# Kernel tuning notes

Hardware: AMD Instinct MI355X
Metric: run time of the kernel (lower is better)

The kernel has to match this reference:

```python
import jax, jax.numpy as jnp
import numpy as np

EPS = 1e-5
N_HEADS = 4

def _ln(x, s, b):
    m = x.mean(-1, keepdims=True)
    v = ((x - m) ** 2).mean(-1, keepdims=True)
    return (x - m) / jnp.sqrt(v + EPS) * s + b

def _gelu(x):
    return jax.nn.gelu(x, approximate=False)  # torch nn.GELU default (erf)


def setup_inputs() -> dict:
    key = jax.random.key(0)
    ks = jax.random.split(key, 20)
    H, AF, BF, DEPTH = 256, 153, 14, 4
    n_mols, apm = 1024, 48
    n_atoms = n_mols * apm          # 49152
    max_nb = 6
    n_bonds = 3 * n_atoms           # 147456 directed bonds
    def nrm(k, shape, scale=0.02):
        return jax.random.normal(k, shape, jnp.float32) * scale
    return dict(
        f_atoms=jax.random.normal(ks[0], (n_atoms, AF), jnp.float32),
        f_bonds=jax.random.normal(ks[1], (n_bonds, BF), jnp.float32),
        a2b=jax.random.randint(ks[2], (n_atoms, max_nb), 0, n_bonds),
        b2a=jax.random.randint(ks[3], (n_bonds,), 0, n_atoms),
        b2revb=jax.random.randint(ks[4], (n_bonds,), 0, n_bonds),
        W_i=nrm(ks[5], (AF + BF, H)), b_i=jnp.zeros((H,), jnp.float32),
        W_h=nrm(ks[6], (DEPTH - 1, H, H)), b_h=jnp.zeros((DEPTH - 1, H), jnp.float32),
        ln_msg_s=jnp.ones((DEPTH - 1, H), jnp.float32), ln_msg_b=jnp.zeros((DEPTH - 1, H), jnp.float32),
        W_o=nrm(ks[7], (AF + H, H)), b_o=jnp.zeros((H,), jnp.float32),
        ln_atom_s=jnp.ones((H,), jnp.float32), ln_atom_b=jnp.zeros((H,), jnp.float32),
        q_w=nrm(ks[8], (H, H)), q_b=jnp.zeros((H,), jnp.float32),
        k_w=nrm(ks[9], (H, H)), k_b=jnp.zeros((H,), jnp.float32),
        v_w=nrm(ks[10], (H, H)), v_b=jnp.zeros((H,), jnp.float32),
        o_w=nrm(ks[11], (H, H)), o_b=jnp.zeros((H,), jnp.float32),
        ln1_s=jnp.ones((H,), jnp.float32), ln1_b=jnp.zeros((H,), jnp.float32),
        ln2_s=jnp.ones((H,), jnp.float32), ln2_b=jnp.zeros((H,), jnp.float32),
        ff1_w=nrm(ks[12], (H, 2 * H)), ff1_b=jnp.zeros((2 * H,), jnp.float32),
        ff2_w=nrm(ks[13], (2 * H, H)), ff2_b=jnp.zeros((H,), jnp.float32),
        readout_query=nrm(ks[14], (1, 1, H)),
        rk_w=nrm(ks[15], (H, H)), rk_b=jnp.zeros((H,), jnp.float32),
        n_mols=n_mols, atoms_per_mol=apm,
    )


def reference(f_atoms, f_bonds, a2b, b2a, b2revb,
              W_i, b_i, W_h, b_h, ln_msg_s, ln_msg_b, W_o, b_o,
              ln_atom_s, ln_atom_b, q_w, q_b, k_w, k_b, v_w, v_b, o_w, o_b,
              ln1_s, ln1_b, ln2_s, ln2_b, ff1_w, ff1_b, ff2_w, ff2_b,
              readout_query, rk_w, rk_b, n_mols, atoms_per_mol):
    H = W_i.shape[1]
    HD = H // N_HEADS
    depth = W_h.shape[0] + 1

    # ---- D-MPNN message passing over directed bonds ----
    message = _gelu(jnp.concatenate([f_atoms[b2a], f_bonds], axis=1) @ W_i + b_i)  # [n_bonds,H]
    for t in range(depth - 1):  # fixed small depth loop
        nei = message[a2b].sum(axis=1)                 # [n_atoms,H] gather-sum over incoming bonds
        nei_m = nei[b2a] - message[b2revb]             # [n_bonds,H] subtract reverse bond
        message = message + _gelu(_ln(nei_m, ln_msg_s[t], ln_msg_b[t]) @ W_h[t] + b_h[t])

    a_message = message[a2b].sum(axis=1)               # [n_atoms,H]
    atom_h = _gelu(jnp.concatenate([f_atoms, a_message], axis=1) @ W_o + b_o)
    atom_h = _ln(atom_h, ln_atom_s, ln_atom_b)

    # uniform scopes: padding loop becomes a reshape, mask is all-valid
    x = atom_h.reshape(n_mols, atoms_per_mol, H)

    # ---- pre-norm TransformerEncoderLayer ----
    h = _ln(x, ln1_s, ln1_b)
    def heads(t):
        return t.reshape(n_mols, atoms_per_mol, N_HEADS, HD).transpose(0, 2, 1, 3)
    q = heads(h @ q_w + q_b)
    k = heads(h @ k_w + k_b)
    v = heads(h @ v_w + v_b)
    attn = jax.nn.softmax(jnp.einsum('bhqd,bhkd->bhqk', q, k) / float(np.sqrt(HD)), axis=-1)
    ctx = jnp.einsum('bhqk,bhkd->bhqd', attn, v).transpose(0, 2, 1, 3).reshape(n_mols, atoms_per_mol, H)
    x = x + (ctx @ o_w + o_b)
    h2 = _ln(x, ln2_s, ln2_b)
    x = x + (_gelu(h2 @ ff1_w + ff1_b) @ ff2_w + ff2_b)

    # ---- attention-weighted readout ----
    keys = x @ rk_w + rk_b                             # [B,S,H]
    scores = jnp.einsum('bsh,h->bs', keys, readout_query[0, 0])
    w = jax.nn.softmax(scores, axis=-1)[..., None]
    return (x * w).sum(axis=1)                         # [B,H]
```

## Files before the change

kernel.cpp:

```cpp
#include <hip/hip_runtime.h>
#include <hip/hip_bf16.h>
#include <math.h>

#define H 256
#define AFEAT 153
#define BFEAT 14
#define KINIT 167
#define NA 49152
#define NB 147456
#define NMOL 1024
#define APM 48
#define MAXNB 6
#define NHEAD 4
#define HDIM 64
#define EPSLN 1e-5f
#define KI_PAD 192
#define KO_PAD 448

typedef unsigned short u16;
typedef __attribute__((ext_vector_type(8))) short bf16x8;
typedef __attribute__((ext_vector_type(4))) short bf16x4;
typedef __attribute__((ext_vector_type(4))) float f32x4;

__device__ __forceinline__ float gelu_f(float x) {
    return 0.5f * x * (1.0f + erff(x * 0.70710678118654752f));
}
__device__ __forceinline__ float wave_sum(float v) {
    #pragma unroll
    for (int m = 1; m < 64; m <<= 1) v += __shfl_xor(v, m);
    return v;
}
__device__ __forceinline__ float b2f(u16 u) {
    union { unsigned u32; float f; } c; c.u32 = ((unsigned)u) << 16; return c.f;
}
__device__ __forceinline__ u16 f2b(float f) {
    __hip_bfloat16 h = __float2bfloat16(f);
    u16 u; __builtin_memcpy(&u, &h, 2); return u;
}
__device__ __forceinline__ ushort4 f2b4(float a, float b, float c, float d) {
    ushort4 o; o.x = f2b(a); o.y = f2b(b); o.z = f2b(c); o.w = f2b(d); return o;
}
__device__ __forceinline__ unsigned addbf2(unsigned a, unsigned b) {
    float lo = b2f((u16)(a & 0xffff)) + b2f((u16)(b & 0xffff));
    float hi = b2f((u16)(a >> 16)) + b2f((u16)(b >> 16));
    return ((unsigned)f2b(hi) << 16) | (unsigned)f2b(lo);
}
__device__ __forceinline__ uint4 addbf8(uint4 a, uint4 b) {
    uint4 r;
    r.x = addbf2(a.x, b.x); r.y = addbf2(a.y, b.y);
    r.z = addbf2(a.z, b.z); r.w = addbf2(a.w, b.w);
    return r;
}

__device__ __forceinline__ f32x4 mfma16(bf16x4 a, bf16x4 b, f32x4 c) {
#if __has_builtin(__builtin_amdgcn_mfma_f32_16x16x16bf16_1k)
    return __builtin_amdgcn_mfma_f32_16x16x16bf16_1k(a, b, c, 0, 0, 0);
#elif __has_builtin(__builtin_amdgcn_mfma_f32_16x16x16_bf16_1k)
    return __builtin_amdgcn_mfma_f32_16x16x16_bf16_1k(a, b, c, 0, 0, 0);
#elif __has_builtin(__builtin_amdgcn_mfma_f32_16x16x16_bf16)
    return __builtin_amdgcn_mfma_f32_16x16x16_bf16(a, b, c, 0, 0, 0);
#else
    f32x4 d;
    asm("v_mfma_f32_16x16x16_bf16 %0, %1, %2, %3"
        : "=&v"(d) : "v"(a), "v"(b), "v"(c));
    return d;
#endif
}

typedef const __attribute__((address_space(1))) void* gas_ptr;
typedef __attribute__((address_space(3))) void* las_ptr;
__device__ __forceinline__ void gload_lds16(const u16* g, u16* l) {
    __builtin_amdgcn_global_load_lds((gas_ptr)g, (las_ptr)l, 16, 0, 0);
}

template<bool GELU, bool ACCUM>
__global__ __launch_bounds__(256) void gemm_mfma_k(
    const u16* __restrict__ A, int Ka,
    const u16* __restrict__ Wt,
    const float* __restrict__ bias,
    u16* __restrict__ C, int Nc, int K)
{
    __shared__ __align__(16) u16 S[128 * 128];
    u16* As = S;
    u16* Bs = S + 8192;
    const int tid = threadIdx.x;
    const int w = tid >> 6, l = tid & 63;
    const int r0 = blockIdx.x * 128;
    const int cb0 = blockIdx.y * 128;
    const int wr = (w >> 1) * 64;
    const int wc = (w & 1) * 64;

    f32x4 acc[4][4];
    #pragma unroll
    for (int m = 0; m < 4; ++m)
        #pragma unroll
        for (int n = 0; n < 4; ++n) acc[m][n] = (f32x4){0.f, 0.f, 0.f, 0.f};

    const int srow = l >> 3;
    const int ssrc = ((l & 7) * 16) ^ (srow << 4);
    const int fr = l & 15;
    const int fh = l >> 4;
    const int swz = (fr & 7) << 4;

    for (int k0 = 0; k0 < K; k0 += 64) {
        #pragma unroll
        for (int i = 0; i < 4; ++i) {
            const int seg = w * 4 + i;
            gload_lds16(A + (size_t)(r0 + seg * 8 + srow) * Ka + k0 + (ssrc >> 1),
                        &As[seg * 512]);
            gload_lds16(Wt + (size_t)(cb0 + seg * 8 + srow) * Ka + k0 + (ssrc >> 1),
                        &Bs[seg * 512]);
        }
        __syncthreads();
        #pragma unroll
        for (int s = 0; s < 2; ++s) {
            const int cbyte = ((s * 64 + fh * 16) ^ swz) >> 1;
            bf16x8 af[4], bv[4];
            #pragma unroll
            for (int m = 0; m < 4; ++m)
                af[m] = *(const bf16x8*)&As[(wr + m * 16 + fr) * 64 + cbyte];
            #pragma unroll
            for (int n = 0; n < 4; ++n)
                bv[n] = *(const bf16x8*)&Bs[(wc + n * 16 + fr) * 64 + cbyte];
            #pragma unroll
            for (int m = 0; m < 4; ++m)
                #pragma unroll
                for (int n = 0; n < 4; ++n)
                    acc[m][n] = __builtin_amdgcn_mfma_f32_16x16x32_bf16(
                        af[m], bv[n], acc[m][n], 0, 0, 0);
        }
        __syncthreads();
    }

    float bvv[4];
    #pragma unroll
    for (int n = 0; n < 4; ++n) bvv[n] = bias[cb0 + wc + n * 16 + fr];
    #pragma unroll
    for (int m = 0; m < 4; ++m)
        #pragma unroll
        for (int n = 0; n < 4; ++n) {
            const int col = wc + n * 16 + fr;
            #pragma unroll
            for (int j = 0; j < 4; ++j) {
                const int row = wr + m * 16 + fh * 4 + j;
                float v = acc[m][n][j] + bvv[n];
                if (GELU) v = gelu_f(v);
                *(u16*)((char*)S + row * 256 + ((col * 2) ^ ((row & 7) << 4))) = f2b(v);
            }
        }
    __syncthreads();
    {
        const int rrow = tid >> 1;
        const int rch = (tid & 1) * 128;
        const int rswz = (rrow & 7) << 4;
        u16* gp = C + (size_t)(r0 + rrow) * Nc + cb0 + (tid & 1) * 64;
        #pragma unroll
        for (int q = 0; q < 8; ++q) {
            uint4 dv = *(const uint4*)((const char*)S + rrow * 256 + ((rch + q * 16) ^ rswz));
            if (ACCUM) {
                uint4 ov = *(const uint4*)(gp + q * 8);
                dv = addbf8(dv, ov);
            }
            *(uint4*)(gp + q * 8) = dv;
        }
    }
}

struct LGather {
    const u16* nei; const u16* msg; const int* b2a; const int* b2revb;
    __device__ __forceinline__ float4 load4(int row, int lane) const {
        const int a = b2a[row], rv = b2revb[row];
        ushort4 un = *(const ushort4*)(nei + (size_t)a * H + lane * 4);
        ushort4 um = *(const ushort4*)(msg + (size_t)rv * H + lane * 4);
        return make_float4(b2f(un.x) - b2f(um.x), b2f(un.y) - b2f(um.y),
                           b2f(un.z) - b2f(um.z), b2f(un.w) - b2f(um.w));
    }
};
struct LPlain {
    const u16* X;
    __device__ __forceinline__ float4 load4(int row, int lane) const {
        ushort4 u = *(const ushort4*)(X + (size_t)row * H + lane * 4);
        return make_float4(b2f(u.x), b2f(u.y), b2f(u.z), b2f(u.w));
    }
};

template<class L, bool GELU, bool ACCUM>
__global__ __launch_bounds__(512, 4) void fln_gemm_k(
    L ld, const u16* __restrict__ Wt,
    const float* __restrict__ lns, const float* __restrict__ lnb,
    const float* __restrict__ bias,
    const u16* __restrict__ Cold,
    u16* __restrict__ C, int Nc)
{
    __shared__ __align__(16) u16 SH[64 * 256 + 256 * 64];
    u16* Alds = SH;
    u16* Blds = SH + 64 * 256;
    const int tid = threadIdx.x;
    const int w = tid >> 6, l = tid & 63;
    const int r0 = blockIdx.x * 64;
    const int cb0 = blockIdx.y * 256;
    const int fr = l & 15, fh = l >> 4;
    const int swzf = (fr & 7) << 4;

    {
        float4 sv = *(const float4*)(lns + l * 4);
        float4 bv = *(const float4*)(lnb + l * 4);
        #pragma unroll
        for (int i = 0; i < 8; ++i) {
            const int r = w * 8 + i;
            float4 v = ld.load4(r0 + r, l);
            float mean = wave_sum(v.x + v.y + v.z + v.w) * (1.0f / H);
            float dx = v.x - mean, dy = v.y - mean, dz = v.z - mean, dw = v.w - mean;
            float var = wave_sum(dx * dx + dy * dy + dz * dz + dw * dw) * (1.0f / H);
            float inv = rsqrtf(var + EPSLN);
            ushort4 o = f2b4(dx * inv * sv.x + bv.x, dy * inv * sv.y + bv.y,
                             dz * inv * sv.z + bv.z, dw * inv * sv.w + bv.w);
            *(ushort4*)((char*)&Alds[(size_t)r * 256] + ((l * 8) ^ ((r & 7) << 4))) = o;
        }
    }

    f32x4 acc[2][4];
    #pragma unroll
    for (int m = 0; m < 2; ++m)
        #pragma unroll
        for (int n = 0; n < 4; ++n) acc[m][n] = (f32x4){0.f, 0.f, 0.f, 0.f};

    const int wr = (w >> 2) * 32;
    const int wc = (w & 3) * 64;

    for (int kk = 0; kk < 4; ++kk) {
        #pragma unroll
        for (int i = 0; i < 4; ++i) {
            const int seg = w * 4 + i;
            const int n = seg * 8 + (l >> 3);
            const int sb = ((l & 7) * 16) ^ ((n & 7) << 4);
            gload_lds16(Wt + (size_t)(cb0 + n) * H + kk * 64 + (sb >> 1),
                        &Blds[seg * 512]);
        }
        __syncthreads();
        #pragma unroll
        for (int s = 0; s < 2; ++s) {
            bf16x8 af[2], bv[4];
            #pragma unroll
            for (int m = 0; m < 2; ++m)
                af[m] = *(const bf16x8*)((const char*)&Alds[(size_t)(wr + m * 16 + fr) * 256]
                        + ((kk * 128 + s * 64 + fh * 16) ^ swzf));
            #pragma unroll
            for (int n = 0; n < 4; ++n)
                bv[n] = *(const bf16x8*)((const char*)&Blds[(size_t)(wc + n * 16 + fr) * 64]
                        + ((s * 64 + fh * 16) ^ swzf));
            #pragma unroll
            for (int m = 0; m < 2; ++m)
                #pragma unroll
                for (int n = 0; n < 4; ++n)
                    acc[m][n] = __builtin_amdgcn_mfma_f32_16x16x32_bf16(
                        af[m], bv[n], acc[m][n], 0, 0, 0);
        }
        __syncthreads();
    }

    float bvv[4];
    #pragma unroll
    for (int n = 0; n < 4; ++n) bvv[n] = bias[cb0 + wc + n * 16 + fr];
    #pragma unroll
    for (int m = 0; m < 2; ++m)
        #pragma unroll
        for (int n = 0; n < 4; ++n) {
            const int col = wc + n * 16 + fr;
            #pragma unroll
            for (int j = 0; j < 4; ++j) {
                const int row = wr + m * 16 + fh * 4 + j;
                float v = acc[m][n][j] + bvv[n];
                if (GELU) v = gelu_f(v);
                *(u16*)((char*)&Alds[(size_t)row * 256] + ((col * 2) ^ ((row & 7) << 4))) = f2b(v);
            }
        }
    __syncthreads();
    {
        const int rrow = tid >> 3;
        const int rch = (tid & 7) * 64;
        const int rswz = (rrow & 7) << 4;
        u16* gp = C + (size_t)(r0 + rrow) * Nc + cb0 + (tid & 7) * 32;
        const u16* op = Cold + (size_t)(r0 + rrow) * Nc + cb0 + (tid & 7) * 32;
        #pragma unroll
        for (int q = 0; q < 4; ++q) {
            uint4 dv = *(const uint4*)((const char*)&Alds[(size_t)rrow * 256]
                        + ((rch + q * 16) ^ rswz));
            if (ACCUM) {
                uint4 ov = *(const uint4*)(op + q * 8);
                dv = addbf8(dv, ov);
            }
            *(uint4*)(gp + q * 8) = dv;
        }
    }
}

__global__ __launch_bounds__(256) void wcvt_k(const float* __restrict__ W,
    u16* __restrict__ Wt, int K, int N, int Kpad)
{
    int idx = blockIdx.x * 256 + threadIdx.x;
    if (idx >= N * Kpad) return;
    int n = idx / Kpad, kp = idx - n * Kpad;
    Wt[idx] = (kp < K) ? f2b(W[(size_t)kp * N + n]) : (u16)0;
}

__global__ void biaspack_k(const float* q, const float* k, const float* v, float* dst) {
    int t = threadIdx.x;
    dst[t] = q[t]; dst[256 + t] = k[t]; dst[512 + t] = v[t];
}

__global__ __launch_bounds__(256) void ainit_k(const float* __restrict__ fa,
    const float* __restrict__ fb, const int* __restrict__ b2a, u16* __restrict__ dst)
{
    const int w = threadIdx.x >> 6, l = threadIdx.x & 63;
    const int row = blockIdx.x * 4 + w;
    const int a = b2a[row];
    const float* fsrc = fa + (size_t)a * AFEAT;
    u16* d = dst + (size_t)row * KI_PAD;
    #pragma unroll
    for (int i = 0; i < 3; ++i) {
        int c = l + i * 64;
        float v;
        if (c < AFEAT) v = fsrc[c];
        else if (c < KINIT) v = fb[(size_t)row * BFEAT + (c - AFEAT)];
        else v = 0.f;
        d[c] = f2b(v);
    }
}

__global__ __launch_bounds__(256) void acat_k(const float* __restrict__ fa,
    const u16* __restrict__ nei, u16* __restrict__ dst)
{
    const int w = threadIdx.x >> 6, l = threadIdx.x & 63;
    const int row = blockIdx.x * 4 + w;
    const float* fsrc = fa + (size_t)row * AFEAT;
    const u16* nsrc = nei + (size_t)row * H;
    u16* d = dst + (size_t)row * KO_PAD;
    #pragma unroll
    for (int i = 0; i < 7; ++i) {
        int c = l + i * 64;
        u16 v;
        if (c < AFEAT) v = f2b(fsrc[c]);
        else if (c < AFEAT + H) v = nsrc[c - AFEAT];
        else v = 0;
        d[c] = v;
    }
}

__global__ __launch_bounds__(256) void nei_sum_k(const u16* __restrict__ msg,
    const int* __restrict__ a2b, u16* __restrict__ nei)
{
    const int wave = threadIdx.x >> 6;
    const int lane = threadIdx.x & 63;
    const int atom = blockIdx.x * 4 + wave;
    float ax = 0.f, ay = 0.f, az = 0.f, aw = 0.f;
    #pragma unroll
    for (int j = 0; j < MAXNB; ++j) {
        int b = a2b[atom * MAXNB + j];
        ushort4 v = *(const ushort4*)(msg + (size_t)b * H + lane * 4);
        ax += b2f(v.x); ay += b2f(v.y); az += b2f(v.z); aw += b2f(v.w);
    }
    *(ushort4*)(nei + (size_t)atom * H + lane * 4) = f2b4(ax, ay, az, aw);
}

__global__ __launch_bounds__(256) void row_ln_k(const u16* __restrict__ in,
    u16* __restrict__ out, const float* __restrict__ s, const float* __restrict__ b)
{
    const int wave = threadIdx.x >> 6;
    const int lane = threadIdx.x & 63;
    const int row = blockIdx.x * 4 + wave;
    ushort4 u = *(const ushort4*)(in + (size_t)row * H + lane * 4);
    float vx = b2f(u.x), vy = b2f(u.y), vz = b2f(u.z), vw = b2f(u.w);
    float mean = wave_sum(vx + vy + vz + vw) * (1.0f / H);
    float dx = vx - mean, dy = vy - mean, dz = vz - mean, dw = vw - mean;
    float var = wave_sum(dx * dx + dy * dy + dz * dz + dw * dw) * (1.0f / H);
    float inv = rsqrtf(var + EPSLN);
    float4 s4 = *(const float4*)(s + lane * 4);
    float4 b4 = *(const float4*)(b + lane * 4);
    *(ushort4*)(out + (size_t)row * H + lane * 4) =
        f2b4(dx * inv * s4.x + b4.x, dy * inv * s4.y + b4.y,
             dz * inv * s4.z + b4.z, dw * inv * s4.w + b4.w);
}

#define VPAD 268
__global__ __launch_bounds__(256) void attn_mfma_k(const u16* __restrict__ qkv,
    u16* __restrict__ ctx)
{
    __shared__ u16 Vs[48][VPAD];
    const int mol = blockIdx.x;
    const int tid = threadIdx.x;
    const int w = tid >> 6;
    const int l = tid & 63;
    const int fr = l & 15;
    const int fh = l >> 4;
    const size_t qb = (size_t)mol * APM * 768;

    {
        const int r = tid >> 4;
        const int c = (tid & 15) * 16;
        #pragma unroll
        for (int i = 0; i < 3; ++i) {
            const int row = r + i * 16;
            const u16* src = qkv + qb + (size_t)row * 768 + 512 + c;
            ushort4 a0 = *(const ushort4*)(src);
            ushort4 a1 = *(const ushort4*)(src + 4);
            ushort4 a2 = *(const ushort4*)(src + 8);
            ushort4 a3 = *(const ushort4*)(src + 12);
            *(ushort4*)&Vs[row][c]      = a0;
            *(ushort4*)&Vs[row][c + 4]  = a1;
            *(ushort4*)&Vs[row][c + 8]  = a2;
            *(ushort4*)&Vs[row][c + 12] = a3;
        }
    }
    __syncthreads();

    f32x4 st[3][3];
    {
        bf16x8 kf[3][2], qf[3][2];
        #pragma unroll
        for (int t = 0; t < 3; ++t)
            #pragma unroll
            for (int ks = 0; ks < 2; ++ks) {
                const size_t rowb = qb + (size_t)(t * 16 + fr) * 768;
                kf[t][ks] = *(const bf16x8*)(qkv + rowb + 256 + w * 64 + ks * 32 + fh * 8);
                qf[t][ks] = *(const bf16x8*)(qkv + rowb +       w * 64 + ks * 32 + fh * 8);
            }
        #pragma unroll
        for (int mi = 0; mi < 3; ++mi)
            #pragma unroll
            for (int ni = 0; ni < 3; ++ni) {
                f32x4 a = (f32x4){0.f, 0.f, 0.f, 0.f};
                a = __builtin_amdgcn_mfma_f32_16x16x32_bf16(kf[mi][0], qf[ni][0], a, 0, 0, 0);
                a = __builtin_amdgcn_mfma_f32_16x16x32_bf16(kf[mi][1], qf[ni][1], a, 0, 0, 0);
                st[mi][ni] = a;
            }
    }

    float inv_sum[3];
    #pragma unroll
    for (int ni = 0; ni < 3; ++ni) {
        float m = -1e30f;
        #pragma unroll
        for (int mi = 0; mi < 3; ++mi)
            #pragma unroll
            for (int j = 0; j < 4; ++j) m = fmaxf(m, st[mi][ni][j]);
        m = fmaxf(m, __shfl_xor(m, 16));
        m = fmaxf(m, __shfl_xor(m, 32));
        float s = 0.f;
        #pragma unroll
        for (int mi = 0; mi < 3; ++mi)
            #pragma unroll
            for (int j = 0; j < 4; ++j) {
                float e = expf((st[mi][ni][j] - m) * 0.125f);
                st[mi][ni][j] = e;
                s += e;
            }
        s += __shfl_xor(s, 16);
        s += __shfl_xor(s, 32);
        inv_sum[ni] = 1.0f / s;
    }

    bf16x4 pf[3][3];
    #pragma unroll
    for (int mi = 0; mi < 3; ++mi)
        #pragma unroll
        for (int ni = 0; ni < 3; ++ni) {
            bf16x4 p;
            p[0] = (short)f2b(st[mi][ni][0]);
            p[1] = (short)f2b(st[mi][ni][1]);
            p[2] = (short)f2b(st[mi][ni][2]);
            p[3] = (short)f2b(st[mi][ni][3]);
            pf[mi][ni] = p;
        }

    f32x4 co[4][3];
    #pragma unroll
    for (int dt = 0; dt < 4; ++dt)
        #pragma unroll
        for (int ni = 0; ni < 3; ++ni) co[dt][ni] = (f32x4){0.f, 0.f, 0.f, 0.f};
    #pragma unroll
    for (int kt = 0; kt < 3; ++kt) {
        bf16x4 vf[4];
        #pragma unroll
        for (int dt = 0; dt < 4; ++dt) {
            const int colu = w * 64 + dt * 16 + fr;
            bf16x4 t;
            #pragma unroll
            for (int e = 0; e < 4; ++e)
                t[e] = (short)Vs[kt * 16 + fh * 4 + e][colu];
            vf[dt] = t;
        }
        #pragma unroll
        for (int dt = 0; dt < 4; ++dt)
            #pragma unroll
            for (int ni = 0; ni < 3; ++ni)
                co[dt][ni] = mfma16(vf[dt], pf[kt][ni], co[dt][ni]);
    }

    #pragma unroll
    for (int ni = 0; ni < 3; ++ni) {
        const float is = inv_sum[ni];
        u16* rowp = ctx + (size_t)(mol * APM + ni * 16 + fr) * H + w * 64;
        #pragma unroll
        for (int dt = 0; dt < 4; ++dt) {
            *(ushort4*)(rowp + dt * 16 + fh * 4) =
                f2b4(co[dt][ni][0] * is, co[dt][ni][1] * is,
                     co[dt][ni][2] * is, co[dt][ni][3] * is);
        }
    }
}

__global__ __launch_bounds__(256) void readout_prep_k(const float* __restrict__ rk_w,
    const float* __restrict__ rk_b, const float* __restrict__ query, float* __restrict__ small)
{
    __shared__ float qsh[256];
    __shared__ float red[4];
    const int t = threadIdx.x;
    qsh[t] = query[t];
    __syncthreads();
    float acc = 0.f;
    #pragma unroll
    for (int c = 0; c < 256; c += 4) {
        float4 w = *(const float4*)&rk_w[(size_t)t * 256 + c];
        acc += w.x * qsh[c] + w.y * qsh[c+1] + w.z * qsh[c+2] + w.w * qsh[c+3];
    }
    small[t] = acc;
    float term = wave_sum(rk_b[t] * qsh[t]);
    if ((t & 63) == 0) red[t >> 6] = term;
    __syncthreads();
    if (t == 0) small[256] = red[0] + red[1] + red[2] + red[3];
}

__global__ __launch_bounds__(256) void readout_k(const u16* __restrict__ x,
    const float* __restrict__ small, float* __restrict__ out)
{
    __shared__ float sc[48];
    __shared__ float rvs[256];
    const int mol = blockIdx.x;
    const int t = threadIdx.x;
    const int wave = t >> 6, lane = t & 63;
    rvs[t] = small[t];
    __syncthreads();
    const float c0 = small[256];
    const size_t xb = (size_t)mol * APM * H;
    for (int i = 0; i < 12; ++i) {
        int s = wave * 12 + i;
        ushort4 xu = *(const ushort4*)(x + xb + (size_t)s * H + lane * 4);
        float dot = b2f(xu.x) * rvs[lane*4] + b2f(xu.y) * rvs[lane*4+1]
                  + b2f(xu.z) * rvs[lane*4+2] + b2f(xu.w) * rvs[lane*4+3];
        dot = wave_sum(dot);
        if (lane == 0) sc[s] = dot + c0;
    }
    __syncthreads();
    if (wave == 0) {
        float v = (lane < 48) ? sc[lane] : -1e30f;
        float mx = v;
        #pragma unroll
        for (int m = 1; m < 64; m <<= 1) mx = fmaxf(mx, __shfl_xor(mx, m));
        float e = (lane < 48) ? expf(v - mx) : 0.f;
        float sum = wave_sum(e);
        if (lane < 48) sc[lane] = e / sum;
    }
    __syncthreads();
    float acc = 0.f;
    for (int s = 0; s < 48; ++s) acc += sc[s] * b2f(x[xb + (size_t)s * H + t]);
    out[(size_t)mol * H + t] = acc;
}

__global__ void diag_k(float* out, int n, float val) {
    int i = blockIdx.x * 256 + threadIdx.x;
    if (i < n) out[i] = (i == 0) ? val : 0.f;
}

extern "C" void kernel_launch(void* const* d_in, const int* in_sizes, int n_in,
                              void* d_out, int out_size, void* d_ws, size_t ws_size,
                              hipStream_t stream)
{
    const float* f_atoms = (const float*)d_in[0];
    const float* f_bonds = (const float*)d_in[1];
    const int*   a2b     = (const int*)d_in[2];
    const int*   b2a     = (const int*)d_in[3];
    const int*   b2revb  = (const int*)d_in[4];
    const float* W_i = (const float*)d_in[5];
    const float* b_i = (const float*)d_in[6];
    const float* W_h = (const float*)d_in[7];
    const float* b_h = (const float*)d_in[8];
    const float* ln_msg_s = (const float*)d_in[9];
    const float* ln_msg_b = (const float*)d_in[10];
    const float* W_o = (const float*)d_in[11];
    const float* b_o = (const float*)d_in[12];
    const float* ln_atom_s = (const float*)d_in[13];
    const float* ln_atom_b = (const float*)d_in[14];
    const float* q_w = (const float*)d_in[15];
    const float* q_b = (const float*)d_in[16];
    const float* k_w = (const float*)d_in[17];
    const float* k_b = (const float*)d_in[18];
    const float* v_w = (const float*)d_in[19];
    const float* v_b = (const float*)d_in[20];
    const float* o_w = (const float*)d_in[21];
    const float* o_b = (const float*)d_in[22];
    const float* ln1_s = (const float*)d_in[23];
    const float* ln1_b = (const float*)d_in[24];
    const float* ln2_s = (const float*)d_in[25];
    const float* ln2_b = (const float*)d_in[26];
    const float* ff1_w = (const float*)d_in[27];
    const float* ff1_b = (const float*)d_in[28];
    const float* ff2_w = (const float*)d_in[29];
    const float* ff2_b = (const float*)d_in[30];
    const float* rquery = (const float*)d_in[31];
    const float* rk_w = (const float*)d_in[32];
    const float* rk_b = (const float*)d_in[33];

    const size_t SZ_MSG = (size_t)NB * H;
    const size_t SZ_NEI = (size_t)NA * H;
    const size_t W_I_SZ  = 256 * KI_PAD;
    const size_t W_H_SZ  = 3 * 256 * 256;
    const size_t W_O_SZ  = 256 * KO_PAD;
    const size_t W_QKV_SZ = 768 * 256;
    const size_t W_OG_SZ = 256 * 256;
    const size_t W_F1_SZ = 512 * 256;
    const size_t W_F2_SZ = 256 * 512;
    const size_t wtotal = W_I_SZ + W_H_SZ + W_O_SZ + W_QKV_SZ + W_OG_SZ + W_F1_SZ + W_F2_SZ;
    const size_t required = (2 * SZ_MSG + SZ_NEI + wtotal) * 2 + 768 * 4 + 257 * 4 + 256;
    if (ws_size < required) {
        diag_k<<<dim3((out_size + 255) / 256), dim3(256), 0, stream>>>(
            (float*)d_out, out_size, (float)(ws_size >> 20));
        return;
    }

    u16* msgA   = (u16*)d_ws;
    u16* msgB   = msgA + SZ_MSG;
    u16* nei    = msgB + SZ_MSG;
    u16* wt_i   = nei + SZ_NEI;
    u16* wt_h   = wt_i + W_I_SZ;
    u16* wt_o   = wt_h + W_H_SZ;
    u16* wt_qkv = wt_o + W_O_SZ;
    u16* wt_og  = wt_qkv + W_QKV_SZ;
    u16* wt_f1  = wt_og + W_OG_SZ;
    u16* wt_f2  = wt_f1 + W_F1_SZ;
    float* qkvb = (float*)(wt_f2 + W_F2_SZ);
    float* small = qkvb + 768;
    float* out = (float*)d_out;

    dim3 blk(256);
    dim3 blk5(512);
    #define WCVT(W, DST, K, N, KP) wcvt_k<<<dim3(((N)*(KP)+255)/256), blk, 0, stream>>>(W, DST, K, N, KP)

    WCVT(W_i, wt_i, KINIT, 256, KI_PAD);
    WCVT(W_h,           wt_h,           256, 256, 256);
    WCVT(W_h + 65536,   wt_h + 65536,   256, 256, 256);
    WCVT(W_h + 131072,  wt_h + 131072,  256, 256, 256);
    WCVT(W_o, wt_o, AFEAT + H, 256, KO_PAD);
    WCVT(q_w, wt_qkv,          256, 256, 256);
    WCVT(k_w, wt_qkv + 65536,  256, 256, 256);
    WCVT(v_w, wt_qkv + 131072, 256, 256, 256);
    WCVT(o_w, wt_og, 256, 256, 256);
    WCVT(ff1_w, wt_f1, 256, 512, 256);
    WCVT(ff2_w, wt_f2, 512, 256, 512);
    biaspack_k<<<dim3(1), blk, 0, stream>>>(q_b, k_b, v_b, qkvb);

    ainit_k<<<dim3(NB / 4), blk, 0, stream>>>(f_atoms, f_bonds, b2a, msgB);
    gemm_mfma_k<true, false><<<dim3(NB / 128, 2), blk, 0, stream>>>(
        msgB, KI_PAD, wt_i, b_i, msgA, H, KI_PAD);

    u16* cur = msgA;
    u16* oth = msgB;
    for (int t = 0; t < 3; ++t) {
        nei_sum_k<<<dim3(NA / 4), blk, 0, stream>>>(cur, a2b, nei);
        fln_gemm_k<LGather, true, true><<<dim3(NB / 64, 1), blk5, 0, stream>>>(
            LGather{nei, cur, b2a, b2revb}, wt_h + (size_t)t * 65536,
            ln_msg_s + t * H, ln_msg_b + t * H, b_h + t * H,
            cur, oth, H);
        u16* tmp = cur; cur = oth; oth = tmp;
    }

    nei_sum_k<<<dim3(NA / 4), blk, 0, stream>>>(cur, a2b, nei);
    acat_k<<<dim3(NA / 4), blk, 0, stream>>>(f_atoms, nei, oth);
    u16* x = cur;
    gemm_mfma_k<true, false><<<dim3(NA / 128, 2), blk, 0, stream>>>(
        oth, KO_PAD, wt_o, b_o, x, H, KO_PAD);
    row_ln_k<<<dim3(NA / 4), blk, 0, stream>>>(x, x, ln_atom_s, ln_atom_b);

    u16* qkv = oth;
    fln_gemm_k<LPlain, false, false><<<dim3(NA / 64, 3), blk5, 0, stream>>>(
        LPlain{x}, wt_qkv, ln1_s, ln1_b, qkvb, x, qkv, 768);
    u16* ctx = nei;
    attn_mfma_k<<<dim3(NMOL), blk, 0, stream>>>(qkv, ctx);
    gemm_mfma_k<false, true><<<dim3(NA / 128, 2), blk, 0, stream>>>(
        ctx, H, wt_og, o_b, x, H, H);
    u16* ff1o = oth;
    fln_gemm_k<LPlain, true, false><<<dim3(NA / 64, 2), blk5, 0, stream>>>(
        LPlain{x}, wt_f1, ln2_s, ln2_b, ff1_b, x, ff1o, 512);
    gemm_mfma_k<false, true><<<dim3(NA / 128, 2), blk, 0, stream>>>(
        ff1o, 512, wt_f2, ff2_b, x, H, 512);

    readout_prep_k<<<dim3(1), blk, 0, stream>>>(rk_w, rk_b, rquery, small);
    readout_k<<<dim3(NMOL), blk, 0, stream>>>(x, small, out);
}
```

Baseline: 736.0 us.

## Double-buffer weight tiles, widen LN loads, prefetch residual, use fast GELU/exp

The fused LayerNorm+GEMM kernel now double-buffers 32-wide weight K-slices in LDS, so the next slice's global-to-LDS load overlaps the current MFMA step. The LN prologue switches to 16-element vector loads per lane and a single-pass sum/sum-of-squares reduction over 16 lanes. The residual read for the accumulate path is moved ahead of the GEMM. Exact erf GELU is replaced by a tanh-form approximation via __expf and rcp, and softmax exps use __expf, trading some accuracy for fewer instructions.

```diff
diff --git a/kernel.cpp b/kernel.cpp
--- a/kernel.cpp
+++ b/kernel.cpp
@@ -23,7 +23,13 @@
 typedef __attribute__((ext_vector_type(4))) float f32x4;
 
 __device__ __forceinline__ float gelu_f(float x) {
-    return 0.5f * x * (1.0f + erff(x * 0.70710678118654752f));
+    float t = -1.5957691216f * x * (1.0f + 0.044715f * x * x);
+    float e = __expf(t);
+#if __has_builtin(__builtin_amdgcn_rcpf)
+    return x * __builtin_amdgcn_rcpf(1.0f + e);
+#else
+    return x / (1.0f + e);
+#endif
 }
 __device__ __forceinline__ float wave_sum(float v) {
     #pragma unroll
@@ -32,6 +38,12 @@
 }
 __device__ __forceinline__ float b2f(u16 u) {
     union { unsigned u32; float f; } c; c.u32 = ((unsigned)u) << 16; return c.f;
+}
+__device__ __forceinline__ float blo(unsigned w) {
+    union { unsigned u; float f; } c; c.u = w << 16; return c.f;
+}
+__device__ __forceinline__ float bhi(unsigned w) {
+    union { unsigned u; float f; } c; c.u = w & 0xffff0000u; return c.f;
 }
 __device__ __forceinline__ u16 f2b(float f) {
     __hip_bfloat16 h = __float2bfloat16(f);
@@ -39,6 +51,10 @@
 }
 __device__ __forceinline__ ushort4 f2b4(float a, float b, float c, float d) {
     ushort4 o; o.x = f2b(a); o.y = f2b(b); o.z = f2b(c); o.w = f2b(d); return o;
+}
+__device__ __forceinline__ void up8(uint4 u, float* v) {
+    v[0]=blo(u.x); v[1]=bhi(u.x); v[2]=blo(u.y); v[3]=bhi(u.y);
+    v[4]=blo(u.z); v[5]=bhi(u.z); v[6]=blo(u.w); v[7]=bhi(u.w);
 }
 __device__ __forceinline__ unsigned addbf2(unsigned a, unsigned b) {
     float lo = b2f((u16)(a & 0xffff)) + b2f((u16)(b & 0xffff));
@@ -168,19 +184,22 @@
 
 struct LGather {
     const u16* nei; const u16* msg; const int* b2a; const int* b2revb;
-    __device__ __forceinline__ float4 load4(int row, int lane) const {
+    __device__ __forceinline__ void load16(int row, int g, float* v) const {
         const int a = b2a[row], rv = b2revb[row];
-        ushort4 un = *(const ushort4*)(nei + (size_t)a * H + lane * 4);
-        ushort4 um = *(const ushort4*)(msg + (size_t)rv * H + lane * 4);
-        return make_float4(b2f(un.x) - b2f(um.x), b2f(un.y) - b2f(um.y),
-                           b2f(un.z) - b2f(um.z), b2f(un.w) - b2f(um.w));
+        const uint4* np = (const uint4*)(nei + (size_t)a * H + g * 16);
+        const uint4* mp = (const uint4*)(msg + (size_t)rv * H + g * 16);
+        float nv[16], mv[16];
+        up8(np[0], nv); up8(np[1], nv + 8);
+        up8(mp[0], mv); up8(mp[1], mv + 8);
+        #pragma unroll
+        for (int j = 0; j < 16; ++j) v[j] = nv[j] - mv[j];
     }
 };
 struct LPlain {
     const u16* X;
-    __device__ __forceinline__ float4 load4(int row, int lane) const {
-        ushort4 u = *(const ushort4*)(X + (size_t)row * H + lane * 4);
-        return make_float4(b2f(u.x), b2f(u.y), b2f(u.z), b2f(u.w));
+    __device__ __forceinline__ void load16(int row, int g, float* v) const {
+        const uint4* p = (const uint4*)(X + (size_t)row * H + g * 16);
+        up8(p[0], v); up8(p[1], v + 8);
     }
 };
 
@@ -192,9 +211,10 @@
     const u16* __restrict__ Cold,
     u16* __restrict__ C, int Nc)
 {
-    __shared__ __align__(16) u16 SH[64 * 256 + 256 * 64];
+    __shared__ __align__(16) u16 SH[64 * 256 + 2 * 256 * 32];
     u16* Alds = SH;
-    u16* Blds = SH + 64 * 256;
+    u16* Bbuf0 = SH + 16384;
+    u16* Bbuf1 = SH + 16384 + 8192;
     const int tid = threadIdx.x;
     const int w = tid >> 6, l = tid & 63;
     const int r0 = blockIdx.x * 64;
@@ -202,20 +222,60 @@
     const int fr = l & 15, fh = l >> 4;
     const int swzf = (fr & 7) << 4;
 
+    uint4 oldv[4];
+    if (ACCUM) {
+        const u16* op = Cold + (size_t)(r0 + (tid >> 3)) * Nc + cb0 + (tid & 7) * 32;
+        #pragma unroll
+        for (int q = 0; q < 4; ++q) oldv[q] = *(const uint4*)(op + q * 8);
+    }
+
+    #define STAGE_B(BB, KK) do {                                               \
+        _Pragma("unroll")                                                      \
+        for (int j_ = 0; j_ < 2; ++j_) {                                       \
+            const int seg_ = w * 2 + j_;                                       \
+            const int n_ = seg_ * 16 + (l >> 2);                               \
+            const int u_ = (n_ & 3) ^ ((n_ >> 2) & 3);                         \
+            gload_lds16(Wt + (size_t)(cb0 + n_) * H + (KK) * 32                \
+                        + (((l & 3) ^ u_) << 3), (BB) + seg_ * 512);           \
+        }                                                                      \
+    } while (0)
+    STAGE_B(Bbuf0, 0);
+
     {
-        float4 sv = *(const float4*)(lns + l * 4);
-        float4 bv = *(const float4*)(lnb + l * 4);
-        #pragma unroll
-        for (int i = 0; i < 8; ++i) {
-            const int r = w * 8 + i;
-            float4 v = ld.load4(r0 + r, l);
-            float mean = wave_sum(v.x + v.y + v.z + v.w) * (1.0f / H);
-            float dx = v.x - mean, dy = v.y - mean, dz = v.z - mean, dw = v.w - mean;
-            float var = wave_sum(dx * dx + dy * dy + dz * dz + dw * dw) * (1.0f / H);
-            float inv = rsqrtf(var + EPSLN);
-            ushort4 o = f2b4(dx * inv * sv.x + bv.x, dy * inv * sv.y + bv.y,
-                             dz * inv * sv.z + bv.z, dw * inv * sv.w + bv.w);
-            *(ushort4*)((char*)&Alds[(size_t)r * 256] + ((l * 8) ^ ((r & 7) << 4))) = o;
+        const int g = l & 15;
+        float4 sv[4], bb[4];
+        #pragma unroll
+        for (int q = 0; q < 4; ++q) {
+            sv[q] = *(const float4*)(lns + g * 16 + q * 4);
+            bb[q] = *(const float4*)(lnb + g * 16 + q * 4);
+        }
+        #pragma unroll
+        for (int i = 0; i < 2; ++i) {
+            const int r = w * 8 + i * 4 + (l >> 4);
+            float v[16];
+            ld.load16(r0 + r, g, v);
+            float s = 0.f, s2 = 0.f;
+            #pragma unroll
+            for (int j = 0; j < 16; ++j) { s += v[j]; s2 = fmaf(v[j], v[j], s2); }
+            #pragma unroll
+            for (int m = 1; m < 16; m <<= 1) {
+                s += __shfl_xor(s, m);
+                s2 += __shfl_xor(s2, m);
+            }
+            const float mean = s * (1.0f / H);
+            const float var = fmaxf(s2 * (1.0f / H) - mean * mean, 0.f);
+            const float inv = rsqrtf(var + EPSLN);
+            const int swr = (r & 7) << 4;
+            #pragma unroll
+            for (int q = 0; q < 4; ++q) {
+                const float* sq = (const float*)&sv[q];
+                const float* bq = (const float*)&bb[q];
+                ushort4 o = f2b4((v[q*4+0]-mean)*inv*sq[0] + bq[0],
+                                 (v[q*4+1]-mean)*inv*sq[1] + bq[1],
+                                 (v[q*4+2]-mean)*inv*sq[2] + bq[2],
+                                 (v[q*4+3]-mean)*inv*sq[3] + bq[3]);
+                *(ushort4*)((char*)Alds + r * 512 + ((g * 32 + q * 8) ^ swr)) = o;
+            }
         }
     }
 
@@ -228,36 +288,32 @@
     const int wr = (w >> 2) * 32;
     const int wc = (w & 3) * 64;
 
-    for (int kk = 0; kk < 4; ++kk) {
-        #pragma unroll
-        for (int i = 0; i < 4; ++i) {
-            const int seg = w * 4 + i;
-            const int n = seg * 8 + (l >> 3);
-            const int sb = ((l & 7) * 16) ^ ((n & 7) << 4);
-            gload_lds16(Wt + (size_t)(cb0 + n) * H + kk * 64 + (sb >> 1),
-                        &Blds[seg * 512]);
-        }
+    __syncthreads();
+
+    #pragma unroll
+    for (int kk = 0; kk < 8; ++kk) {
+        if (kk < 7) STAGE_B((kk & 1) ? Bbuf0 : Bbuf1, kk + 1);
+        const u16* Bb = (kk & 1) ? Bbuf1 : Bbuf0;
+        bf16x8 af[2], bv[4];
+        #pragma unroll
+        for (int m = 0; m < 2; ++m)
+            af[m] = *(const bf16x8*)((const char*)Alds + (wr + m * 16 + fr) * 512
+                    + ((kk * 64 + fh * 16) ^ swzf));
+        #pragma unroll
+        for (int n = 0; n < 4; ++n) {
+            const int nc = wc + n * 16 + fr;
+            const int u = (nc & 3) ^ ((nc >> 2) & 3);
+            bv[n] = *(const bf16x8*)((const char*)Bb + nc * 64 + ((fh ^ u) << 4));
+        }
+        #pragma unroll
+        for (int m = 0; m < 2; ++m)
+            #pragma unroll
+            for (int n = 0; n < 4; ++n)
+                acc[m][n] = __builtin_amdgcn_mfma_f32_16x16x32_bf16(
+                    af[m], bv[n], acc[m][n], 0, 0, 0);
         __syncthreads();
-        #pragma unroll
-        for (int s = 0; s < 2; ++s) {
-            bf16x8 af[2], bv[4];
-            #pragma unroll
-            for (int m = 0; m < 2; ++m)
-                af[m] = *(const bf16x8*)((const char*)&Alds[(size_t)(wr + m * 16 + fr) * 256]
-                        + ((kk * 128 + s * 64 + fh * 16) ^ swzf));
-            #pragma unroll
-            for (int n = 0; n < 4; ++n)
-                bv[n] = *(const bf16x8*)((const char*)&Blds[(size_t)(wc + n * 16 + fr) * 64]
-                        + ((s * 64 + fh * 16) ^ swzf));
-            #pragma unroll
-            for (int m = 0; m < 2; ++m)
-                #pragma unroll
-                for (int n = 0; n < 4; ++n)
-                    acc[m][n] = __builtin_amdgcn_mfma_f32_16x16x32_bf16(
-                        af[m], bv[n], acc[m][n], 0, 0, 0);
-        }
-        __syncthreads();
-    }
+    }
+    #undef STAGE_B
 
     float bvv[4];
     #pragma unroll
@@ -272,7 +328,7 @@
                 const int row = wr + m * 16 + fh * 4 + j;
                 float v = acc[m][n][j] + bvv[n];
                 if (GELU) v = gelu_f(v);
-                *(u16*)((char*)&Alds[(size_t)row * 256] + ((col * 2) ^ ((row & 7) << 4))) = f2b(v);
+                *(u16*)((char*)Alds + row * 512 + ((col * 2) ^ ((row & 7) << 4))) = f2b(v);
             }
         }
     __syncthreads();
@@ -281,15 +337,10 @@
         const int rch = (tid & 7) * 64;
         const int rswz = (rrow & 7) << 4;
         u16* gp = C + (size_t)(r0 + rrow) * Nc + cb0 + (tid & 7) * 32;
-        const u16* op = Cold + (size_t)(r0 + rrow) * Nc + cb0 + (tid & 7) * 32;
         #pragma unroll
         for (int q = 0; q < 4; ++q) {
-            uint4 dv = *(const uint4*)((const char*)&Alds[(size_t)rrow * 256]
-                        + ((rch + q * 16) ^ rswz));
-            if (ACCUM) {
-                uint4 ov = *(const uint4*)(op + q * 8);
-                dv = addbf8(dv, ov);
-            }
+            uint4 dv = *(const uint4*)((const char*)Alds + rrow * 512 + ((rch + q * 16) ^ rswz));
+            if (ACCUM) dv = addbf8(dv, oldv[q]);
             *(uint4*)(gp + q * 8) = dv;
         }
     }
@@ -451,7 +502,7 @@
         for (int mi = 0; mi < 3; ++mi)
             #pragma unroll
             for (int j = 0; j < 4; ++j) {
-                float e = expf((st[mi][ni][j] - m) * 0.125f);
+                float e = __expf((st[mi][ni][j] - m) * 0.125f);
                 st[mi][ni][j] = e;
                 s += e;
             }
@@ -557,7 +608,7 @@
         float mx = v;
         #pragma unroll
         for (int m = 1; m < 64; m <<= 1) mx = fmaxf(mx, __shfl_xor(mx, m));
-        float e = (lane < 48) ? expf(v - mx) : 0.f;
+        float e = (lane < 48) ? __expf(v - mx) : 0.f;
         float sum = wave_sum(e);
         if (lane < 48) sc[lane] = e / sum;
     }
```

After: 734.5 us. Within noise of the previous version (-0.2%).
